# Performance work log

Measured on AMD Instinct MI355X. Metric: run time of the kernel, lower is better.

## Reference

```python
import jax, jax.numpy as jnp
import numpy as np

N = 50000      # n_points (== n_support, non-strided)
H = 32         # neighbors per point
IN_F = 128
OUT_F = 256
MID = OUT_F // 4   # bottleneck width = 64
K = 15         # kernel points
RADIUS = 2.0
KP_EXTENT = 1.2 * RADIUS / 5.0  # config.KP_extent * radius / density_parameter
EPS = 1e-6
SLOPE = 0.1


def _wvar(k, size):
    # weight_variable: normal(scale=sqrt(2/size[-1])), zeroed outside 2*std
    std = np.sqrt(2.0 / size[-1])
    w = jax.random.normal(k, size, jnp.float32) * std
    return jnp.where(jnp.abs(w) > 2.0 * std, 0.0, w)


def setup_inputs():
    key = jax.random.key(0)
    ks = jax.random.split(key, 12)
    query_points = jax.random.uniform(ks[0], (N, 3), jnp.float32)
    support_points = query_points  # non-strided: same cloud
    neighbors_indices = jax.random.randint(ks[1], (N, H), 0, N, jnp.int32)
    features = jax.random.normal(ks[2], (N, IN_F), jnp.float32)
    kp = (jax.random.uniform(ks[3], (K, 3), jnp.float32) * 2.0 - 1.0) * (0.66 * KP_EXTENT)
    kernel_points = kp.at[0].set(0.0)  # fixed_kernel_points='center'
    w1 = _wvar(ks[4], (IN_F, MID))
    kw = _wvar(ks[5], (K, MID, MID))
    w3 = _wvar(ks[6], (MID, OUT_F))
    ws = _wvar(ks[7], (IN_F, OUT_F))
    def bnp(k, c):
        k1, k2 = jax.random.split(k)
        g = jax.random.uniform(k1, (c,), jnp.float32, 0.75, 1.25)
        b = jax.random.normal(k2, (c,), jnp.float32) * 0.1
        return g, b
    g1, b1 = bnp(ks[8], MID)
    g2, b2 = bnp(ks[9], MID)
    g3, b3 = bnp(ks[10], OUT_F)
    gs, bs = bnp(ks[11], OUT_F)
    return dict(query_points=query_points, support_points=support_points,
                neighbors_indices=neighbors_indices, features=features,
                kernel_points=kernel_points, w1=w1, g1=g1, b1=b1,
                kw=kw, g2=g2, b2=b2, w3=w3, g3=g3, b3=b3, ws=ws, gs=gs, bs=bs)


def _bn(x, g, b):
    # BatchNorm1d in training mode: batch statistics over points, biased var
    m = jnp.mean(x, 0)
    v = jnp.var(x, 0)
    return g * (x - m) * jax.lax.rsqrt(v + EPS) + b


def _lrelu(x):
    return jnp.where(x >= 0, x, SLOPE * x)


def _unary(x, w, g, b):
    return _lrelu(_bn(x @ w, g, b))


def _kpconv(q, s, inds, f, kp, kw):
    # pad support with a far shadow point and features with a zero row (faithful to KPConv)
    s_pad = jnp.concatenate([s, jnp.full((1, 3), 1e6, s.dtype)], 0)
    f_pad = jnp.concatenate([f, jnp.zeros((1, f.shape[1]), f.dtype)], 0)
    neigh = s_pad[inds]                        # [n,h,3] gather
    d = neigh - q[:, None, :]                  # [n,h,3]
    sq = jnp.sum((d[:, :, None, :] - kp[None, None, :, :]) ** 2, -1)  # [n,h,K]
    dist = jnp.sqrt(jnp.maximum(sq, 1e-12))
    infl = jnp.maximum(0.0, 1.0 - dist / KP_EXTENT)   # 'linear' KP_influence
    nf = f_pad[inds]                           # [n,h,d] gather
    wf = jnp.einsum('nhk,nhd->nkd', infl, nf)  # aggregate over neighbors
    return jnp.einsum('nkd,kdo->no', wf, kw)   # 'sum' aggregation over kernel pts


def reference(query_points, support_points, neighbors_indices, features, kernel_points,
              w1, g1, b1, kw, g2, b2, w3, g3, b3, ws, gs, bs):
    x = _unary(features, w1, g1, b1)                                     # conv1
    x = _lrelu(_bn(_kpconv(query_points, support_points, neighbors_indices,
                           x, kernel_points, kw), g2, b2))               # conv2 (KPConv)
    x = _unary(x, w3, g3, b3)                                            # conv3
    sc = _unary(features, ws, gs, bs)                                    # shortcut (non-strided)
    return _lrelu(sc + x)
```

## Files before the change

### kernel.cpp

```cpp
#include <hip/hip_runtime.h>

#define NPTS 50000
#define HN 32
#define INF1 128
#define OUTF3 256
#define MIDF 64
#define KP 15
#define EPSV 1e-6f
#define SLOPE 0.1f
#define KPE 0.48f
#define INVN (1.f / 50000.f)

typedef __attribute__((ext_vector_type(8))) short short8;
typedef __attribute__((ext_vector_type(4))) float float4v;
typedef unsigned short ushort;
typedef unsigned long long ull;

__device__ inline ushort f2bf(float f) {
    union { float f; unsigned u; } v; v.f = f;
    unsigned r = v.u + 0x7fff + ((v.u >> 16) & 1);
    return (ushort)(r >> 16);
}
__device__ inline float bf2f(ushort u) {
    union { unsigned u; float f; } v; v.u = ((unsigned)u) << 16;
    return v.f;
}

__device__ inline void repack_one(const float* W, ushort* Wp, int K, int N, int lid) {
    int l  = lid & 63;
    int NT = N / 16;
    int nt = (lid >> 6) % NT;
    int s  = lid / (64 * NT);
    int n  = nt * 16 + (l & 15);
    int k0 = s * 32 + ((l >> 4) & 3) * 8;
#pragma unroll
    for (int j = 0; j < 8; j++)
        Wp[lid * 8 + j] = f2bf(W[(k0 + j) * N + n]);
}

__global__ __launch_bounds__(256)
void k_repack_all(const float* __restrict__ w1, ushort* __restrict__ wp1,
                  const float* __restrict__ kw, ushort* __restrict__ wpk,
                  const float* __restrict__ w3, ushort* __restrict__ wp3,
                  const float* __restrict__ wsw, ushort* __restrict__ wpS) {
    int id = blockIdx.x * 256 + threadIdx.x;
    if (id < 1024)        repack_one(w1,  wp1, INF1,      MIDF,  id);
    else if (id < 8704)   repack_one(kw,  wpk, KP * MIDF, MIDF,  id - 1024);
    else if (id < 10752)  repack_one(w3,  wp3, MIDF,      OUTF3, id - 8704);
    else if (id < 14848)  repack_one(wsw, wpS, INF1,      OUTF3, id - 10752);
}

template<int K, int N, bool A16, bool C16, bool STATS>
__global__ __launch_bounds__(256)
void k_gemm(const ushort* __restrict__ Ab, const float* __restrict__ Af,
            const ushort* __restrict__ Wp,
            float* __restrict__ Cf, ushort* __restrict__ Cb,
            float* __restrict__ Sa, float* __restrict__ Sq, int M) {
    constexpr int KSTEPS = K / 32;
    constexpr int NT = N / 16;
    __shared__ float sred[N], qred[N];
    int t = threadIdx.x;
    int w = t >> 6, l = t & 63;

    if (STATS) {
        for (int c = t; c < N; c += 256) { sred[c] = 0.f; qred[c] = 0.f; }
        __syncthreads();
    }

    int m0 = blockIdx.x * 64 + w * 16;
    int row = m0 + (l & 15);
    long arow = (row < M) ? row : (M - 1);
    int aoff = (l >> 4) * 8;
    const short8* Bp = (const short8*)Wp + l;

    float4v acc[NT];
#pragma unroll
    for (int j = 0; j < NT; j++) acc[j] = (float4v){0.f, 0.f, 0.f, 0.f};

#pragma unroll
    for (int s = 0; s < KSTEPS; s++) {
        short8 af;
        if (A16) {
            af = *(const short8*)(Ab + arow * K + aoff + s * 32);
        } else {
            const float* ap = Af + arow * K + aoff + s * 32;
            float4 a0 = *(const float4*)(ap);
            float4 a1 = *(const float4*)(ap + 4);
            union { short8 v; ushort u[8]; } au;
            au.u[0] = f2bf(a0.x); au.u[1] = f2bf(a0.y); au.u[2] = f2bf(a0.z); au.u[3] = f2bf(a0.w);
            au.u[4] = f2bf(a1.x); au.u[5] = f2bf(a1.y); au.u[6] = f2bf(a1.z); au.u[7] = f2bf(a1.w);
            af = au.v;
        }
#pragma unroll
        for (int j = 0; j < NT; j++) {
            short8 bf = Bp[(s * NT + j) * 64];
            acc[j] = __builtin_amdgcn_mfma_f32_16x16x32_bf16(af, bf, acc[j], 0, 0, 0);
        }
    }

    int col = l & 15;
    int rb = (l >> 4) * 4;
#pragma unroll
    for (int r = 0; r < 4; r++) {
        int rr = m0 + rb + r;
        if (rr < M) {
#pragma unroll
            for (int j = 0; j < NT; j++) {
                if (C16) Cb[(long)rr * N + j * 16 + col] = f2bf(acc[j][r]);
                else     Cf[(long)rr * N + j * 16 + col] = acc[j][r];
            }
        }
    }

    if (STATS) {
#pragma unroll
        for (int j = 0; j < NT; j++) {
            float s = 0.f, q = 0.f;
#pragma unroll
            for (int r = 0; r < 4; r++) {
                float v = ((m0 + rb + r) < M) ? acc[j][r] : 0.f;
                s += v; q += v * v;
            }
            s += __shfl_xor(s, 16); s += __shfl_xor(s, 32);
            q += __shfl_xor(q, 16); q += __shfl_xor(q, 32);
            if ((l >> 4) == 0) {
                atomicAdd(&sred[j * 16 + col], s);
                atomicAdd(&qred[j * 16 + col], q);
            }
        }
        __syncthreads();
        for (int c = t; c < N; c += 256) {
            atomicAdd(&Sa[c], sred[c]);
            atomicAdd(&Sq[c], qred[c]);
        }
    }
}

__global__ __launch_bounds__(256)
void k_bnx(const ushort* __restrict__ X, ushort* __restrict__ Y,
           const float* __restrict__ Sa, const float* __restrict__ Sq,
           const float* __restrict__ g, const float* __restrict__ b) {
    __shared__ float sc[64], sh[64];
    int t = threadIdx.x;
    if (t < 64) {
        float m = Sa[t] * INVN;
        float v = Sq[t] * INVN - m * m;
        float s = g[t] * rsqrtf(v + EPSV);
        sc[t] = s; sh[t] = b[t] - s * m;
    }
    __syncthreads();
    long i = (long)(blockIdx.x * 256 + t) * 4;
    ull vin = *(const ull*)(X + i);
    int c0 = (int)(i & 63);
    ull vout = 0;
#pragma unroll
    for (int j = 0; j < 4; j++) {
        float f = bf2f((ushort)((vin >> (16 * j)) & 0xffff));
        float v = f * sc[c0 + j] + sh[c0 + j];
        v = (v >= 0.f) ? v : SLOPE * v;
        vout |= ((ull)f2bf(v)) << (16 * j);
    }
    *(ull*)(Y + i) = vout;
}

__global__ __launch_bounds__(256)
void k_kpconv(const float* __restrict__ qpts, const float* __restrict__ spts,
              const int* __restrict__ nbr, const ushort* __restrict__ x1b,
              const float* __restrict__ kpp, const ushort* __restrict__ kwp,
              ushort* __restrict__ y, float* __restrict__ Sa, float* __restrict__ Sq) {
    __shared__ __align__(16) ushort wfs[16][968];
    __shared__ float posd[4][3][HN];
    __shared__ int   sidx[4][HN];

    int t = threadIdx.x;
    int w = t >> 6, l = t & 63;
    int dl = l & 15;
    int q4 = l >> 4;

    int kq = dl;
    int kmin = (kq < 15) ? kq : 14;
    float kx = kpp[kmin * 3 + 0], ky = kpp[kmin * 3 + 1], kz = kpp[kmin * 3 + 2];

    for (int pp = 0; pp < 4; pp++) {
        int p = w * 4 + pp;
        int n = blockIdx.x * 16 + p;

        if (l < HN) {
            int idx = nbr[n * HN + l];
            sidx[w][l] = idx;
            float qx = qpts[n * 3 + 0], qy = qpts[n * 3 + 1], qz = qpts[n * 3 + 2];
            posd[w][0][l] = spts[idx * 3 + 0] - qx;
            posd[w][1][l] = spts[idx * 3 + 1] - qy;
            posd[w][2][l] = spts[idx * 3 + 2] - qz;
        }

        union { short8 v; ushort u[8]; } afr;
#pragma unroll
        for (int j = 0; j < 8; j++) {
            int h = q4 * 8 + j;
            float ex = posd[w][0][h] - kx;
            float ey = posd[w][1][h] - ky;
            float ez = posd[w][2][h] - kz;
            float sq = ex * ex + ey * ey + ez * ez;
            float dist = sqrtf(fmaxf(sq, 1e-12f));
            float inf = fmaxf(0.f, 1.f - dist * (1.f / KPE));
            afr.u[j] = (kq < 15) ? f2bf(inf) : (ushort)0;
        }

        int ridx[8];
#pragma unroll
        for (int j = 0; j < 8; j++) ridx[j] = sidx[w][q4 * 8 + j] * MIDF;
        union { short8 v; ushort u[8]; } bfr[4];
#pragma unroll
        for (int nt = 0; nt < 4; nt++)
#pragma unroll
            for (int j = 0; j < 8; j++)
                bfr[nt].u[j] = x1b[ridx[j] + nt * 16 + dl];

        float4v wfacc[4];
#pragma unroll
        for (int nt = 0; nt < 4; nt++)
            wfacc[nt] = __builtin_amdgcn_mfma_f32_16x16x32_bf16(
                afr.v, bfr[nt].v, (float4v){0.f, 0.f, 0.f, 0.f}, 0, 0, 0);

#pragma unroll
        for (int ntx = 0; ntx < 4; ntx++) {
            int nt = (ntx + q4) & 3;
#pragma unroll
            for (int r = 0; r < 4; r++) {
                int k = q4 * 4 + r;
                if (k < 15)
                    wfs[p][k * 64 + nt * 16 + dl] = f2bf(wfacc[nt][r]);
            }
        }
    }
    __syncthreads();

    float4v acc = (float4v){0.f, 0.f, 0.f, 0.f};
    const ushort* arow = &wfs[dl][0] + q4 * 8;
    const short8* Bp = (const short8*)kwp + l;
#pragma unroll 6
    for (int s = 0; s < 30; s++) {
        short8 af = *(const short8*)(arow + s * 32);
        short8 bf = Bp[(s * 4 + w) * 64];
        acc = __builtin_amdgcn_mfma_f32_16x16x32_bf16(af, bf, acc, 0, 0, 0);
    }

    int o = w * 16 + dl;
    float s = 0.f, q = 0.f;
#pragma unroll
    for (int r = 0; r < 4; r++) {
        float v = acc[r];
        y[(long)(blockIdx.x * 16 + q4 * 4 + r) * MIDF + o] = f2bf(v);
        s += v; q += v * v;
    }
    s += __shfl_xor(s, 16); s += __shfl_xor(s, 32);
    q += __shfl_xor(q, 16); q += __shfl_xor(q, 32);
    if (q4 == 0) {
        atomicAdd(&Sa[o], s);
        atomicAdd(&Sq[o], q);
    }
}

__global__ __launch_bounds__(256)
void k_final(const float* __restrict__ x3, float* __restrict__ out,
             const float* __restrict__ a3, const float* __restrict__ q3,
             const float* __restrict__ g3, const float* __restrict__ b3,
             const float* __restrict__ aS, const float* __restrict__ qS,
             const float* __restrict__ gs, const float* __restrict__ bs) {
    __shared__ float s3[256], h3[256], sS[256], hS[256];
    int t = threadIdx.x;
    {
        float m = a3[t] * INVN;
        float v = q3[t] * INVN - m * m;
        float s = g3[t] * rsqrtf(v + EPSV);
        s3[t] = s; h3[t] = b3[t] - s * m;
        m = aS[t] * INVN;
        v = qS[t] * INVN - m * m;
        s = gs[t] * rsqrtf(v + EPSV);
        sS[t] = s; hS[t] = bs[t] - s * m;
    }
    __syncthreads();
    long i = (long)(blockIdx.x * 256 + t) * 4;
    int c0 = (int)(i & 255);
    float4 a = *(const float4*)(x3 + i);
    float4 o = *(const float4*)(out + i);
    float va[4] = {a.x, a.y, a.z, a.w};
    float vo[4] = {o.x, o.y, o.z, o.w};
#pragma unroll
    for (int j = 0; j < 4; j++) {
        int c = c0 + j;
        float x = va[j] * s3[c] + h3[c];
        x = (x >= 0.f) ? x : SLOPE * x;
        float sc = vo[j] * sS[c] + hS[c];
        sc = (sc >= 0.f) ? sc : SLOPE * sc;
        float v = x + sc;
        va[j] = (v >= 0.f) ? v : SLOPE * v;
    }
    *(float4*)(out + i) = (float4){va[0], va[1], va[2], va[3]};
}

extern "C" void kernel_launch(void* const* d_in, const int* in_sizes, int n_in,
                              void* d_out, int out_size, void* d_ws, size_t ws_size,
                              hipStream_t stream) {
    const float* qp   = (const float*)d_in[0];
    const float* sp   = (const float*)d_in[1];
    const int*   nbr  = (const int*)d_in[2];
    const float* feat = (const float*)d_in[3];
    const float* kpp  = (const float*)d_in[4];
    const float* w1   = (const float*)d_in[5];
    const float* g1   = (const float*)d_in[6];
    const float* b1   = (const float*)d_in[7];
    const float* kw   = (const float*)d_in[8];
    const float* g2   = (const float*)d_in[9];
    const float* b2   = (const float*)d_in[10];
    const float* w3   = (const float*)d_in[11];
    const float* g3   = (const float*)d_in[12];
    const float* b3   = (const float*)d_in[13];
    const float* wsw  = (const float*)d_in[14];
    const float* gs   = (const float*)d_in[15];
    const float* bs   = (const float*)d_in[16];
    float* out = (float*)d_out;

    char* base = (char*)d_ws;
    float*  x3    = (float*)base;
    ushort* x1raw = (ushort*)base;
    ushort* x1b   = (ushort*)(base + 6400000);
    ushort* x2raw = (ushort*)(base + 12800000);
    ushort* x2b   = (ushort*)(base + 51200000);
    ushort* wp1   = (ushort*)(base + 57600000);
    ushort* wpk   = (ushort*)(base + 57616384);
    ushort* wp3   = (ushort*)(base + 57739264);
    ushort* wpS   = (ushort*)(base + 57772032);
    float*  st    = (float*)(base + 57837568);
    float* acc1 = st, *q1 = st + 64;
    float* acc2 = st + 128, *q2 = st + 192;
    float* acc3 = st + 256, *q3 = st + 512;
    float* accS = st + 768, *qS = st + 1024;

    hipMemsetAsync(st, 0, 1152 * sizeof(float), stream);

    k_repack_all<<<58, 256, 0, stream>>>(w1, wp1, kw, wpk, w3, wp3, wsw, wpS);

    k_gemm<INF1, MIDF, false, true, true><<<782, 256, 0, stream>>>(
        nullptr, feat, wp1, nullptr, x1raw, acc1, q1, NPTS);
    k_bnx<<<3125, 256, 0, stream>>>(x1raw, x1b, acc1, q1, g1, b1);

    k_kpconv<<<NPTS / 16, 256, 0, stream>>>(qp, sp, nbr, x1b, kpp, wpk, x2raw, acc2, q2);
    k_bnx<<<3125, 256, 0, stream>>>(x2raw, x2b, acc2, q2, g2, b2);

    k_gemm<MIDF, OUTF3, true, false, true><<<782, 256, 0, stream>>>(
        x2b, nullptr, wp3, x3, nullptr, acc3, q3, NPTS);

    k_gemm<INF1, OUTF3, false, false, true><<<782, 256, 0, stream>>>(
        nullptr, feat, wpS, out, nullptr, accS, qS, NPTS);

    k_final<<<12500, 256, 0, stream>>>(x3, out, acc3, q3, g3, b3, accS, qS, gs, bs);
}
```

Baseline: 355.9 us.

## Fuse conv1 with shortcut GEMM, fold BN2 into conv3, stage gathers in LDS

Conv1 and shortcut GEMMs are merged into one kernel that reads features once against a concatenated 64+256-column weight. The BN2+LeakyReLU pass is folded into conv3's A-operand load, which removes one elementwise kernel and its intermediate buffer. Conv3 and shortcut outputs are now stored in bf16 instead of fp32, halving that traffic in the final kernel at some precision cost. In kpconv, neighbor feature rows are gathered with vectorized loads into shared memory before being read as MFMA operands, replacing scalar strided global reads.

Result: faster. 326.7 us (-8.2%).

```diff
diff --git a/kernel.cpp b/kernel.cpp
--- a/kernel.cpp
+++ b/kernel.cpp
@@ -39,39 +39,48 @@
 }
 
 __global__ __launch_bounds__(256)
-void k_repack_all(const float* __restrict__ w1, ushort* __restrict__ wp1,
+void k_repack_all(const float* __restrict__ w1, const float* __restrict__ wsw,
+                  ushort* __restrict__ wpC,
                   const float* __restrict__ kw, ushort* __restrict__ wpk,
-                  const float* __restrict__ w3, ushort* __restrict__ wp3,
-                  const float* __restrict__ wsw, ushort* __restrict__ wpS) {
+                  const float* __restrict__ w3, ushort* __restrict__ wp3) {
     int id = blockIdx.x * 256 + threadIdx.x;
-    if (id < 1024)        repack_one(w1,  wp1, INF1,      MIDF,  id);
-    else if (id < 8704)   repack_one(kw,  wpk, KP * MIDF, MIDF,  id - 1024);
-    else if (id < 10752)  repack_one(w3,  wp3, MIDF,      OUTF3, id - 8704);
-    else if (id < 14848)  repack_one(wsw, wpS, INF1,      OUTF3, id - 10752);
-}
-
-template<int K, int N, bool A16, bool C16, bool STATS>
-__global__ __launch_bounds__(256)
-void k_gemm(const ushort* __restrict__ Ab, const float* __restrict__ Af,
-            const ushort* __restrict__ Wp,
-            float* __restrict__ Cf, ushort* __restrict__ Cb,
-            float* __restrict__ Sa, float* __restrict__ Sq, int M) {
-    constexpr int KSTEPS = K / 32;
-    constexpr int NT = N / 16;
-    __shared__ float sred[N], qred[N];
+    if (id < 5120) {
+        int l  = id & 63;
+        int nt = (id >> 6) % 20;
+        int s  = id / 1280;
+        int n  = nt * 16 + (l & 15);
+        int k0 = s * 32 + ((l >> 4) & 3) * 8;
+#pragma unroll
+        for (int j = 0; j < 8; j++) {
+            float v = (n < 64) ? w1[(k0 + j) * 64 + n] : wsw[(k0 + j) * 256 + (n - 64)];
+            wpC[id * 8 + j] = f2bf(v);
+        }
+    } else if (id < 12800) {
+        repack_one(kw, wpk, KP * MIDF, MIDF, id - 5120);
+    } else if (id < 14848) {
+        repack_one(w3, wp3, MIDF, OUTF3, id - 12800);
+    }
+}
+
+__global__ __launch_bounds__(256)
+void k_conv1sc(const float* __restrict__ feat, const ushort* __restrict__ WpC,
+               ushort* __restrict__ x1raw, ushort* __restrict__ scb,
+               float* __restrict__ Sa1, float* __restrict__ Sq1,
+               float* __restrict__ SaS, float* __restrict__ SqS, int M) {
+    constexpr int KSTEPS = 4, NT = 20;
+    __shared__ float sred[320], qred[320];
     int t = threadIdx.x;
     int w = t >> 6, l = t & 63;
-
-    if (STATS) {
-        for (int c = t; c < N; c += 256) { sred[c] = 0.f; qred[c] = 0.f; }
-        __syncthreads();
-    }
+    int dl = l & 15, q4 = l >> 4;
+
+    for (int c = t; c < 320; c += 256) { sred[c] = 0.f; qred[c] = 0.f; }
+    __syncthreads();
 
     int m0 = blockIdx.x * 64 + w * 16;
-    int row = m0 + (l & 15);
+    int row = m0 + dl;
     long arow = (row < M) ? row : (M - 1);
-    int aoff = (l >> 4) * 8;
-    const short8* Bp = (const short8*)Wp + l;
+    const float* ap0 = feat + arow * INF1 + q4 * 8;
+    const short8* Bp = (const short8*)WpC + l;
 
     float4v acc[NT];
 #pragma unroll
@@ -79,60 +88,138 @@
 
 #pragma unroll
     for (int s = 0; s < KSTEPS; s++) {
-        short8 af;
-        if (A16) {
-            af = *(const short8*)(Ab + arow * K + aoff + s * 32);
-        } else {
-            const float* ap = Af + arow * K + aoff + s * 32;
-            float4 a0 = *(const float4*)(ap);
-            float4 a1 = *(const float4*)(ap + 4);
-            union { short8 v; ushort u[8]; } au;
-            au.u[0] = f2bf(a0.x); au.u[1] = f2bf(a0.y); au.u[2] = f2bf(a0.z); au.u[3] = f2bf(a0.w);
-            au.u[4] = f2bf(a1.x); au.u[5] = f2bf(a1.y); au.u[6] = f2bf(a1.z); au.u[7] = f2bf(a1.w);
-            af = au.v;
-        }
+        const float* ap = ap0 + s * 32;
+        float4 a0 = *(const float4*)(ap);
+        float4 a1 = *(const float4*)(ap + 4);
+        union { short8 v; ushort u[8]; } au;
+        au.u[0] = f2bf(a0.x); au.u[1] = f2bf(a0.y); au.u[2] = f2bf(a0.z); au.u[3] = f2bf(a0.w);
+        au.u[4] = f2bf(a1.x); au.u[5] = f2bf(a1.y); au.u[6] = f2bf(a1.z); au.u[7] = f2bf(a1.w);
 #pragma unroll
         for (int j = 0; j < NT; j++) {
             short8 bf = Bp[(s * NT + j) * 64];
-            acc[j] = __builtin_amdgcn_mfma_f32_16x16x32_bf16(af, bf, acc[j], 0, 0, 0);
-        }
-    }
-
-    int col = l & 15;
-    int rb = (l >> 4) * 4;
+            acc[j] = __builtin_amdgcn_mfma_f32_16x16x32_bf16(au.v, bf, acc[j], 0, 0, 0);
+        }
+    }
+
+    int rb = q4 * 4;
 #pragma unroll
     for (int r = 0; r < 4; r++) {
         int rr = m0 + rb + r;
         if (rr < M) {
 #pragma unroll
             for (int j = 0; j < NT; j++) {
-                if (C16) Cb[(long)rr * N + j * 16 + col] = f2bf(acc[j][r]);
-                else     Cf[(long)rr * N + j * 16 + col] = acc[j][r];
+                int c = j * 16 + dl;
+                ushort v = f2bf(acc[j][r]);
+                if (c < 64) x1raw[(long)rr * 64 + c] = v;
+                else        scb[(long)rr * 256 + (c - 64)] = v;
             }
         }
     }
 
-    if (STATS) {
+#pragma unroll
+    for (int j = 0; j < NT; j++) {
+        float s = 0.f, q = 0.f;
+#pragma unroll
+        for (int r = 0; r < 4; r++) {
+            float v = ((m0 + rb + r) < M) ? acc[j][r] : 0.f;
+            s += v; q += v * v;
+        }
+        s += __shfl_xor(s, 16); s += __shfl_xor(s, 32);
+        q += __shfl_xor(q, 16); q += __shfl_xor(q, 32);
+        if (q4 == 0) {
+            atomicAdd(&sred[j * 16 + dl], s);
+            atomicAdd(&qred[j * 16 + dl], q);
+        }
+    }
+    __syncthreads();
+    for (int c = t; c < 320; c += 256) {
+        if (c < 64) { atomicAdd(&Sa1[c], sred[c]); atomicAdd(&Sq1[c], qred[c]); }
+        else        { atomicAdd(&SaS[c - 64], sred[c]); atomicAdd(&SqS[c - 64], qred[c]); }
+    }
+}
+
+__global__ __launch_bounds__(256)
+void k_conv3(const ushort* __restrict__ x2raw, const ushort* __restrict__ Wp,
+             ushort* __restrict__ x3b,
+             const float* __restrict__ Sa2, const float* __restrict__ Sq2,
+             const float* __restrict__ g2, const float* __restrict__ b2,
+             float* __restrict__ Sa3, float* __restrict__ Sq3, int M) {
+    constexpr int NT = 16;
+    __shared__ float sred[256], qred[256];
+    __shared__ float scs[64], shs[64];
+    int t = threadIdx.x;
+    int w = t >> 6, l = t & 63;
+    int dl = l & 15, q4 = l >> 4;
+
+    if (t < 64) {
+        float m = Sa2[t] * INVN;
+        float v = Sq2[t] * INVN - m * m;
+        float s = g2[t] * rsqrtf(v + EPSV);
+        scs[t] = s; shs[t] = b2[t] - s * m;
+    }
+    if (t < 256) { sred[t] = 0.f; qred[t] = 0.f; }
+    __syncthreads();
+
+    int m0 = blockIdx.x * 64 + w * 16;
+    int row = m0 + dl;
+    long arow = (row < M) ? row : (M - 1);
+    const ushort* ap0 = x2raw + arow * MIDF + q4 * 8;
+    const short8* Bp = (const short8*)Wp + l;
+
+    float4v acc[NT];
+#pragma unroll
+    for (int j = 0; j < NT; j++) acc[j] = (float4v){0.f, 0.f, 0.f, 0.f};
+
+#pragma unroll
+    for (int s = 0; s < 2; s++) {
+        union { short8 v; ushort u[8]; } raw;
+        raw.v = *(const short8*)(ap0 + s * 32);
+        const float* scv = &scs[s * 32 + q4 * 8];
+        const float* shv = &shs[s * 32 + q4 * 8];
+        union { short8 v; ushort u[8]; } au;
+#pragma unroll
+        for (int e = 0; e < 8; e++) {
+            float f = bf2f(raw.u[e]) * scv[e] + shv[e];
+            f = (f >= 0.f) ? f : SLOPE * f;
+            au.u[e] = f2bf(f);
+        }
 #pragma unroll
         for (int j = 0; j < NT; j++) {
-            float s = 0.f, q = 0.f;
-#pragma unroll
-            for (int r = 0; r < 4; r++) {
-                float v = ((m0 + rb + r) < M) ? acc[j][r] : 0.f;
-                s += v; q += v * v;
-            }
-            s += __shfl_xor(s, 16); s += __shfl_xor(s, 32);
-            q += __shfl_xor(q, 16); q += __shfl_xor(q, 32);
-            if ((l >> 4) == 0) {
-                atomicAdd(&sred[j * 16 + col], s);
-                atomicAdd(&qred[j * 16 + col], q);
-            }
-        }
-        __syncthreads();
-        for (int c = t; c < N; c += 256) {
-            atomicAdd(&Sa[c], sred[c]);
-            atomicAdd(&Sq[c], qred[c]);
-        }
+            short8 bf = Bp[(s * NT + j) * 64];
+            acc[j] = __builtin_amdgcn_mfma_f32_16x16x32_bf16(au.v, bf, acc[j], 0, 0, 0);
+        }
+    }
+
+    int rb = q4 * 4;
+#pragma unroll
+    for (int r = 0; r < 4; r++) {
+        int rr = m0 + rb + r;
+        if (rr < M) {
+#pragma unroll
+            for (int j = 0; j < NT; j++)
+                x3b[(long)rr * 256 + j * 16 + dl] = f2bf(acc[j][r]);
+        }
+    }
+
+#pragma unroll
+    for (int j = 0; j < NT; j++) {
+        float s = 0.f, q = 0.f;
+#pragma unroll
+        for (int r = 0; r < 4; r++) {
+            float v = ((m0 + rb + r) < M) ? acc[j][r] : 0.f;
+            s += v; q += v * v;
+        }
+        s += __shfl_xor(s, 16); s += __shfl_xor(s, 32);
+        q += __shfl_xor(q, 16); q += __shfl_xor(q, 32);
+        if (q4 == 0) {
+            atomicAdd(&sred[j * 16 + dl], s);
+            atomicAdd(&qred[j * 16 + dl], q);
+        }
+    }
+    __syncthreads();
+    if (t < 256) {
+        atomicAdd(&Sa3[t], sred[t]);
+        atomicAdd(&Sq3[t], qred[t]);
     }
 }
 
@@ -169,16 +256,16 @@
               const float* __restrict__ kpp, const ushort* __restrict__ kwp,
               ushort* __restrict__ y, float* __restrict__ Sa, float* __restrict__ Sq) {
     __shared__ __align__(16) ushort wfs[16][968];
+    __shared__ __align__(16) ushort fst[4][HN][68];
     __shared__ float posd[4][3][HN];
     __shared__ int   sidx[4][HN];
 
     int t = threadIdx.x;
     int w = t >> 6, l = t & 63;
-    int dl = l & 15;
-    int q4 = l >> 4;
-
-    int kq = dl;
-    int kmin = (kq < 15) ? kq : 14;
+    int dl = l & 15, q4 = l >> 4;
+    int hrow = l >> 3, seg = l & 7;
+
+    int kmin = (dl < 15) ? dl : 14;
     float kx = kpp[kmin * 3 + 0], ky = kpp[kmin * 3 + 1], kz = kpp[kmin * 3 + 2];
 
     for (int pp = 0; pp < 4; pp++) {
@@ -192,6 +279,16 @@
             posd[w][0][l] = spts[idx * 3 + 0] - qx;
             posd[w][1][l] = spts[idx * 3 + 1] - qy;
             posd[w][2][l] = spts[idx * 3 + 2] - qz;
+        }
+
+#pragma unroll
+        for (int c = 0; c < 4; c++) {
+            int h = c * 8 + hrow;
+            long r = (long)sidx[w][h] * MIDF + seg * 8;
+            uint2 d0 = *(const uint2*)(x1b + r);
+            uint2 d1 = *(const uint2*)(x1b + r + 4);
+            *(uint2*)&fst[w][h][seg * 8]     = d0;
+            *(uint2*)&fst[w][h][seg * 8 + 4] = d1;
         }
 
         union { short8 v; ushort u[8]; } afr;
@@ -204,18 +301,15 @@
             float sq = ex * ex + ey * ey + ez * ez;
             float dist = sqrtf(fmaxf(sq, 1e-12f));
             float inf = fmaxf(0.f, 1.f - dist * (1.f / KPE));
-            afr.u[j] = (kq < 15) ? f2bf(inf) : (ushort)0;
-        }
-
-        int ridx[8];
-#pragma unroll
-        for (int j = 0; j < 8; j++) ridx[j] = sidx[w][q4 * 8 + j] * MIDF;
+            afr.u[j] = (dl < 15) ? f2bf(inf) : (ushort)0;
+        }
+
         union { short8 v; ushort u[8]; } bfr[4];
 #pragma unroll
         for (int nt = 0; nt < 4; nt++)
 #pragma unroll
             for (int j = 0; j < 8; j++)
-                bfr[nt].u[j] = x1b[ridx[j] + nt * 16 + dl];
+                bfr[nt].u[j] = fst[w][q4 * 8 + j][nt * 16 + dl];
 
         float4v wfacc[4];
 #pragma unroll
@@ -263,7 +357,8 @@
 }
 
 __global__ __launch_bounds__(256)
-void k_final(const float* __restrict__ x3, float* __restrict__ out,
+void k_final(const ushort* __restrict__ x3b, const ushort* __restrict__ scb,
+             float* __restrict__ out,
              const float* __restrict__ a3, const float* __restrict__ q3,
              const float* __restrict__ g3, const float* __restrict__ b3,
              const float* __restrict__ aS, const float* __restrict__ qS,
@@ -283,21 +378,20 @@
     __syncthreads();
     long i = (long)(blockIdx.x * 256 + t) * 4;
     int c0 = (int)(i & 255);
-    float4 a = *(const float4*)(x3 + i);
-    float4 o = *(const float4*)(out + i);
-    float va[4] = {a.x, a.y, a.z, a.w};
-    float vo[4] = {o.x, o.y, o.z, o.w};
+    ull va = *(const ull*)(x3b + i);
+    ull vb = *(const ull*)(scb + i);
+    float r[4];
 #pragma unroll
     for (int j = 0; j < 4; j++) {
         int c = c0 + j;
-        float x = va[j] * s3[c] + h3[c];
+        float x = bf2f((ushort)((va >> (16 * j)) & 0xffff)) * s3[c] + h3[c];
         x = (x >= 0.f) ? x : SLOPE * x;
-        float sc = vo[j] * sS[c] + hS[c];
+        float sc = bf2f((ushort)((vb >> (16 * j)) & 0xffff)) * sS[c] + hS[c];
         sc = (sc >= 0.f) ? sc : SLOPE * sc;
         float v = x + sc;
-        va[j] = (v >= 0.f) ? v : SLOPE * v;
-    }
-    *(float4*)(out + i) = (float4){va[0], va[1], va[2], va[3]};
+        r[j] = (v >= 0.f) ? v : SLOPE * v;
+    }
+    *(float4*)(out + i) = (float4){r[0], r[1], r[2], r[3]};
 }
 
 extern "C" void kernel_launch(void* const* d_in, const int* in_sizes, int n_in,
@@ -323,37 +417,30 @@
     float* out = (float*)d_out;
 
     char* base = (char*)d_ws;
-    float*  x3    = (float*)base;
-    ushort* x1raw = (ushort*)base;
+    ushort* x1raw = (ushort*)(base + 0);
     ushort* x1b   = (ushort*)(base + 6400000);
     ushort* x2raw = (ushort*)(base + 12800000);
-    ushort* x2b   = (ushort*)(base + 51200000);
-    ushort* wp1   = (ushort*)(base + 57600000);
-    ushort* wpk   = (ushort*)(base + 57616384);
-    ushort* wp3   = (ushort*)(base + 57739264);
-    ushort* wpS   = (ushort*)(base + 57772032);
-    float*  st    = (float*)(base + 57837568);
-    float* acc1 = st, *q1 = st + 64;
+    ushort* x3b   = (ushort*)(base + 19200000);
+    ushort* scb   = (ushort*)(base + 44800000);
+    ushort* wpC   = (ushort*)(base + 70400000);
+    ushort* wpk   = (ushort*)(base + 70481920);
+    ushort* wp3   = (ushort*)(base + 70604800);
+    float*  st    = (float*)(base + 70637568);
+    float* acc1 = st,       *q1 = st + 64;
     float* acc2 = st + 128, *q2 = st + 192;
     float* acc3 = st + 256, *q3 = st + 512;
     float* accS = st + 768, *qS = st + 1024;
 
-    hipMemsetAsync(st, 0, 1152 * sizeof(float), stream);
-
-    k_repack_all<<<58, 256, 0, stream>>>(w1, wp1, kw, wpk, w3, wp3, wsw, wpS);
-
-    k_gemm<INF1, MIDF, false, true, true><<<782, 256, 0, stream>>>(
-        nullptr, feat, wp1, nullptr, x1raw, acc1, q1, NPTS);
+    hipMemsetAsync(st, 0, 1280 * sizeof(float), stream);
+
+    k_repack_all<<<58, 256, 0, stream>>>(w1, wsw, wpC, kw, wpk, w3, wp3);
+
+    k_conv1sc<<<782, 256, 0, stream>>>(feat, wpC, x1raw, scb, acc1, q1, accS, qS, NPTS);
     k_bnx<<<3125, 256, 0, stream>>>(x1raw, x1b, acc1, q1, g1, b1);
 
     k_kpconv<<<NPTS / 16, 256, 0, stream>>>(qp, sp, nbr, x1b, kpp, wpk, x2raw, acc2, q2);
-    k_bnx<<<3125, 256, 0, stream>>>(x2raw, x2b, acc2, q2, g2, b2);
-
-    k_gemm<MIDF, OUTF3, true, false, true><<<782, 256, 0, stream>>>(
-        x2b, nullptr, wp3, x3, nullptr, acc3, q3, NPTS);
-
-    k_gemm<INF1, OUTF3, false, false, true><<<782, 256, 0, stream>>>(
-        nullptr, feat, wpS, out, nullptr, accS, qS, NPTS);
-
-    k_final<<<12500, 256, 0, stream>>>(x3, out, acc3, q3, g3, b3, accS, qS, gs, bs);
-}
+
+    k_conv3<<<782, 256, 0, stream>>>(x2raw, wp3, x3b, acc2, q2, g2, b2, acc3, q3, NPTS);
+
+    k_final<<<12500, 256, 0, stream>>>(x3b, scb, out, acc3, q3, g3, b3, accS, qS, gs, bs);
+}
```
